# Performance work log

Measured on AMD Instinct MI355X. Metric: run time of the kernel, lower is better.

The kernel has to match this reference:

```python
import jax, jax.numpy as jnp
import numpy as np

M_HIST = 5        # Anderson history depth (m=5 in anderson_solver)
N_POWER = 20      # power iterations to estimate sigma for spectral_norm
REG = 1e-4        # Tikhonov regularization on the Anderson LS system
MAX_ITER = 25     # deq_max_iter


def _l2norm(x):
    return x / (jnp.linalg.norm(x) + 1e-12)


def spectral_normalize(W):
    # torch spectral_norm: W / sigma, sigma = u^T W v with u,v from power iteration
    u = _l2norm(jnp.ones((W.shape[0],), W.dtype))
    def body(_, u):
        v = _l2norm(W.T @ u)
        return _l2norm(W @ v)
    u = jax.lax.fori_loop(0, N_POWER, body, u)
    v = _l2norm(W.T @ u)
    u = jax.lax.stop_gradient(u)
    v = jax.lax.stop_gradient(v)
    sigma = u @ (W @ v)
    return W / sigma


def make_f(W1, b1, W2, b2):
    W1s = spectral_normalize(W1)
    W2s = spectral_normalize(W2)
    def f(z, context):
        h = jnp.tanh(jnp.concatenate([z, context], axis=-1) @ W1s.T + b1)
        return jnp.tanh(h @ W2s.T + b2)
    return f


def anderson(f, x0, context, max_iter, m=M_HIST):
    # Mirrors anderson_solver, including its duplicated warm-up step.
    X = [x0]
    F = [f(x0, context)]
    x = F[0]; X.append(x); F.append(f(x, context))
    x = F[0]; X.append(x); F.append(f(x, context))
    for _k in range(2, max_iter):
        m_k = min(len(X) - 1, m)
        dX = jnp.stack([X[-i] - X[-i - 1] for i in range(1, m_k + 1)], axis=-1)  # [B,d,mk]
        dF = jnp.stack([F[-i] - F[-i - 1] for i in range(1, m_k + 1)], axis=-1)
        dG = dF - dX
        A = jnp.einsum('bdi,bdj->bij', dG, dG) + REG * jnp.eye(m_k, dtype=x0.dtype)
        r = F[-1] - X[-1]
        Bv = jnp.einsum('bdi,bd->bi', dG, r)
        alpha = jnp.linalg.solve(A, Bv[..., None])[..., 0]          # [B,mk]
        x = F[-1] - jnp.einsum('bdi,bi->bd', dF, alpha)
        X.append(x)
        F.append(f(x, context))
        if len(X) > m + 1:
            X.pop(0); F.pop(0)
    return X[-1]


def setup_inputs() -> dict:
    key = jax.random.key(0)
    ks = jax.random.split(key, 5)
    B, X_DIM, LATENT, HIDDEN = 2048, 256, 256, 1024
    context = jax.random.normal(ks[0], (B, X_DIM), jnp.float32)
    W1 = jax.random.normal(ks[1], (HIDDEN, LATENT + X_DIM), jnp.float32) / np.sqrt(LATENT + X_DIM)
    b1 = jax.random.normal(ks[2], (HIDDEN,), jnp.float32) * 0.01
    W2 = jax.random.normal(ks[3], (LATENT, HIDDEN), jnp.float32) / np.sqrt(HIDDEN)
    b2 = jax.random.normal(ks[4], (LATENT,), jnp.float32) * 0.01
    return {"context": context, "W1": W1, "b1": b1, "W2": W2, "b2": b2}


def reference(context, W1, b1, W2, b2):
    f = make_f(W1, b1, W2, b2)
    z0 = jnp.zeros((context.shape[0], W2.shape[0]), context.dtype)
    z_star = anderson(f, z0, context, MAX_ITER)
    return z_star
```

## Files before the change

kernel.cpp:

```cpp
#include <hip/hip_runtime.h>
#include <hip/hip_bf16.h>


#define B_ROWS 2048
#define D_LAT  256
#define D_CTX  256
#define D_HID  1024
#define KCAT   512
#define SLOT   (B_ROWS * D_LAT)
#define NRING  7

typedef __bf16 bf16x8 __attribute__((ext_vector_type(8)));
typedef float f32x4 __attribute__((ext_vector_type(4)));
typedef float f32x2 __attribute__((ext_vector_type(2)));
typedef unsigned short u16;

__global__ void init_kernel(const float* __restrict__ ctx,
                            __hip_bfloat16* __restrict__ zc,
                            float* __restrict__ vA, float* __restrict__ uA,
                            float* __restrict__ G1p, float* __restrict__ G2) {
  int i = blockIdx.x * 256 + threadIdx.x;
  if (i < B_ROWS * KCAT) {
    int b = i >> 9, c = i & 511;
    float v = (c < 256) ? 0.0f : ctx[b * 256 + (c - 256)];
    zc[i] = __float2bfloat16(v);
  }
  if (i < 512 * 512) G1p[i] = 0.0f;
  if (i < 256 * 256) G2[i] = 0.0f;
  if (i < KCAT) vA[i] = 0.0f;
  if (i < D_LAT) uA[i] = 1.0f;
}

__global__ __launch_bounds__(256) void gram_kernel(
    const float* __restrict__ W1, const float* __restrict__ W2,
    float* __restrict__ G1p, float* __restrict__ G2) {
  __shared__ float As[32][66];
  __shared__ float Bs[32][34];
  const int tid = threadIdx.x;
  const int tx = tid & 15, ty = tid >> 4;

  const float* X; float* G; int N, ti, tj, k0base; bool modeA;
  int b = blockIdx.x;
  if (b < 1024) {
    modeA = true; X = W1; G = G1p; N = 512;
    int s = b >> 7, t = b & 127;
    ti = t >> 4; tj = t & 15; k0base = s * 128;
  } else {
    modeA = false; b -= 1024; X = W2; G = G2; N = 256;
    int s = b >> 5, t = b & 31;
    ti = t >> 3; tj = t & 7; k0base = s * 128;
  }

  float acc[4][2] = {};
  for (int k0 = k0base; k0 < k0base + 128; k0 += 32) {
    if (modeA) {
      for (int idx = tid; idx < 1024; idx += 256) {
        int r2 = (idx & 31) * 2, c = idx >> 5;
        f32x2 v = *(const f32x2*)(X + (size_t)(k0 + c) * 512 + ti * 64 + r2);
        *(f32x2*)&As[c][r2] = v;
      }
      for (int idx = tid; idx < 512; idx += 256) {
        int r2 = (idx & 15) * 2, c = idx >> 4;
        f32x2 v = *(const f32x2*)(X + (size_t)(k0 + c) * 512 + tj * 32 + r2);
        *(f32x2*)&Bs[c][r2] = v;
      }
    } else {
      for (int idx = tid; idx < 1024; idx += 256) {
        int c2 = (idx & 15) * 2, r = idx >> 4;
        f32x2 v = *(const f32x2*)(X + (size_t)(ti * 64 + r) * 1024 + k0 + c2);
        As[c2][r] = v[0];
        As[c2 + 1][r] = v[1];
      }
      for (int idx = tid; idx < 512; idx += 256) {
        int c2 = (idx & 15) * 2, r = idx >> 4;
        f32x2 v = *(const f32x2*)(X + (size_t)(tj * 32 + r) * 1024 + k0 + c2);
        Bs[c2][r] = v[0];
        Bs[c2 + 1][r] = v[1];
      }
    }
    __syncthreads();
#pragma unroll
    for (int kk = 0; kk < 32; kk++) {
      const float2* ap = (const float2*)&As[kk][ty * 4];
      float2 a0 = ap[0], a1 = ap[1];
      float2 b0 = *(const float2*)&Bs[kk][tx * 2];
      float a[4] = {a0.x, a0.y, a1.x, a1.y};
      float bb[2] = {b0.x, b0.y};
#pragma unroll
      for (int i = 0; i < 4; i++)
#pragma unroll
        for (int j = 0; j < 2; j++) acc[i][j] += a[i] * bb[j];
    }
    __syncthreads();
  }
#pragma unroll
  for (int i = 0; i < 4; i++)
#pragma unroll
    for (int j = 0; j < 2; j++)
      atomicAdd(&G[(size_t)(ti * 64 + ty * 4 + i) * N + tj * 32 + tx * 2 + j],
                acc[i][j]);
}

__global__ __launch_bounds__(256) void colsum_kernel(
    const float* __restrict__ W1, float* __restrict__ vA) {
  int b = blockIdx.x;
  for (int c = threadIdx.x; c < KCAT; c += 256) {
    float s = 0.f;
#pragma unroll
    for (int r = 0; r < 16; r++) s += W1[(size_t)(16 * b + r) * KCAT + c];
    atomicAdd(&vA[c], s);
  }
}

__global__ __launch_bounds__(256) void pmv_kernel(
    const float* __restrict__ G1p, const float* __restrict__ G2,
    const float* __restrict__ vi, float* __restrict__ vo,
    const float* __restrict__ ui, float* __restrict__ uo, int g1_active) {
  int gw = blockIdx.x * 4 + (threadIdx.x >> 6);
  int lane = threadIdx.x & 63;
  const float* G; const float* in; float* out; int n, r;
  if (gw < 512) {
    if (!g1_active) return;
    G = G1p; in = vi; out = vo; n = 512; r = gw;
  } else {
    G = G2; in = ui; out = uo; n = 256; r = gw - 512;
  }
  const float4* Gr = (const float4*)(G + (size_t)r * n);
  const float4* uv = (const float4*)in;
  float acc = 0.f;
  for (int c = lane; c < (n >> 2); c += 64) {
    float4 g = Gr[c], u = uv[c];
    acc += g.x * u.x + g.y * u.y + g.z * u.z + g.w * u.w;
  }
  for (int off = 32; off; off >>= 1) acc += __shfl_down(acc, off, 64);
  if (lane == 0) out[r] = 0.25f * acc;
}

__global__ __launch_bounds__(256) void sigma_kernel(
    const float* __restrict__ vA, const float* __restrict__ vB,
    const float* __restrict__ uA, const float* __restrict__ uB,
    float* __restrict__ sig) {
  float s[4] = {0.f, 0.f, 0.f, 0.f};
  for (int i = threadIdx.x; i < KCAT; i += 256) {
    s[0] += vA[i] * vB[i];
    s[1] += vA[i] * vA[i];
  }
  for (int i = threadIdx.x; i < D_LAT; i += 256) {
    s[2] += uA[i] * uA[i];
    s[3] += uA[i] * uB[i];
  }
  __shared__ float red[4][4];
  int lane = threadIdx.x & 63, w = threadIdx.x >> 6;
  for (int k = 0; k < 4; k++) {
    float a = s[k];
    for (int off = 32; off; off >>= 1) a += __shfl_down(a, off, 64);
    if (lane == 0) red[k][w] = a;
  }
  __syncthreads();
  if (threadIdx.x == 0) {
    float d0 = red[0][0] + red[0][1] + red[0][2] + red[0][3];
    float d1 = red[1][0] + red[1][1] + red[1][2] + red[1][3];
    float d2 = red[2][0] + red[2][1] + red[2][2] + red[2][3];
    float d3 = red[3][0] + red[3][1] + red[3][2] + red[3][3];
    sig[0] = sqrtf(0.25f * d0 / d1);
    sig[1] = sqrtf(0.25f * d2 / d3);
  }
}

__global__ void wfold_kernel(const float* __restrict__ W1,
                             const float* __restrict__ W2,
                             const float* __restrict__ sig,
                             __hip_bfloat16* __restrict__ W1b,
                             __hip_bfloat16* __restrict__ W2b) {
  int i = blockIdx.x * 256 + threadIdx.x;
  if (i < D_HID * KCAT) W1b[i] = __float2bfloat16(W1[i] * sig[0]);
  int j = i - D_HID * KCAT;
  if (j >= 0 && j < D_LAT * D_HID) W2b[j] = __float2bfloat16(W2[j] * sig[1]);
}

__global__ void warm1_kernel(const float* __restrict__ Fh,
                             float* __restrict__ Xh,
                             __hip_bfloat16* __restrict__ zc) {
  int i = blockIdx.x * 256 + threadIdx.x;
  float v = Fh[i];
  Xh[SLOT + i] = v;
  zc[(i >> 8) * KCAT + (i & 255)] = __float2bfloat16(v);
}
__global__ void warm2_kernel(const float* __restrict__ Fh,
                             float* __restrict__ Xh, float* __restrict__ Fw) {
  int i = blockIdx.x * 256 + threadIdx.x;
  Xh[2 * SLOT + i] = Fh[i];
  Fw[2 * SLOT + i] = Fh[SLOT + i];
}

template <int BM, int BN, int K, bool OUT_BF16>
__global__ __launch_bounds__(256) void gemm_mfma(
    const __hip_bfloat16* __restrict__ A, const __hip_bfloat16* __restrict__ W,
    const float* __restrict__ bias, float* __restrict__ Cf,
    __hip_bfloat16* __restrict__ Cb, int N) {
  __shared__ __align__(16) u16 lds[2][(BM + BN) * 64];
  const int tid = threadIdx.x;
  const int lane = tid & 63;
  const int wid = tid >> 6;
  const int wy = wid >> 1, wx = wid & 1;
  constexpr int WM = BM / 2, WN = BN / 2;
  constexpr int MB = WM / 16, NB = WN / 16;
  constexpr int NK = K / 64;
  const int bm = blockIdx.x * BM;
  const int bn = blockIdx.y * BN;
  const int rlo = lane & 15, quad = lane >> 4;

  f32x4 acc[MB][NB] = {};

  auto stage = [&](u16* base, int k0) {
    u16* As = base;
    u16* Ws = base + BM * 64;
    for (int c = tid; c < BM * 8; c += 256) {
      int r = c >> 3, o = (c & 7) ^ (r & 7);
      __builtin_amdgcn_global_load_lds(
          (const __attribute__((address_space(1))) void*)(A + (size_t)(bm + r) * K + k0 + o * 8),
          (__attribute__((address_space(3))) void*)(As + c * 8), 16, 0, 0);
    }
    for (int c = tid; c < BN * 8; c += 256) {
      int r = c >> 3, o = (c & 7) ^ (r & 7);
      __builtin_amdgcn_global_load_lds(
          (const __attribute__((address_space(1))) void*)(W + (size_t)(bn + r) * K + k0 + o * 8),
          (__attribute__((address_space(3))) void*)(Ws + c * 8), 16, 0, 0);
    }
  };
  auto compute = [&](const u16* base) {
    const u16* As = base;
    const u16* Ws = base + BM * 64;
#pragma unroll
    for (int kk = 0; kk < 2; kk++) {
      bf16x8 af[MB], bfr[NB];
#pragma unroll
      for (int mb = 0; mb < MB; mb++) {
        int r = wy * WM + mb * 16 + rlo;
        int o = (kk * 4 + quad) ^ (r & 7);
        af[mb] = *(const bf16x8*)(As + (r * 8 + o) * 8);
      }
#pragma unroll
      for (int nb = 0; nb < NB; nb++) {
        int r = wx * WN + nb * 16 + rlo;
        int o = (kk * 4 + quad) ^ (r & 7);
        bfr[nb] = *(const bf16x8*)(Ws + (r * 8 + o) * 8);
      }
#pragma unroll
      for (int mb = 0; mb < MB; mb++)
#pragma unroll
        for (int nb = 0; nb < NB; nb++)
          acc[mb][nb] = __builtin_amdgcn_mfma_f32_16x16x32_bf16(
              af[mb], bfr[nb], acc[mb][nb], 0, 0, 0);
    }
  };

  stage(&lds[0][0], 0);
  __syncthreads();
#pragma unroll 2
  for (int step = 0; step < NK; step++) {
    u16* cur = (step & 1) ? &lds[1][0] : &lds[0][0];
    u16* nxt = (step & 1) ? &lds[0][0] : &lds[1][0];
    if (step + 1 < NK) stage(nxt, (step + 1) * 64);
    compute(cur);
    if (step + 1 < NK) __syncthreads();
  }

#pragma unroll
  for (int mb = 0; mb < MB; mb++) {
#pragma unroll
    for (int nb = 0; nb < NB; nb++) {
      int n = bn + wx * WN + nb * 16 + rlo;
      float bv = bias[n];
#pragma unroll
      for (int rg = 0; rg < 4; rg++) {
        int m = bm + wy * WM + mb * 16 + quad * 4 + rg;
        float val = tanhf(acc[mb][nb][rg] + bv);
        if constexpr (OUT_BF16) {
          Cb[(size_t)m * N + n] = __float2bfloat16(val);
        } else {
          Cf[(size_t)m * N + n] = val;
        }
      }
    }
  }
}

template <int MK>
__global__ __launch_bounds__(256) void anderson_step_kernel(
    const float* __restrict__ Xh, const float* __restrict__ Fh,
    float* __restrict__ Xw, __hip_bfloat16* __restrict__ zc, int t) {
  const int lane = threadIdx.x & 63;
  const int wid = threadIdx.x >> 6;
  const int b = blockIdx.x * 4 + wid;
  const int base = b * D_LAT + 4 * lane;

  f32x4 f[MK + 1], x[MK + 1];
#pragma unroll
  for (int i = 0; i <= MK; i++) {
    int sl = (t - 1 - i) % NRING;
    f[i] = *(const f32x4*)(Fh + (size_t)sl * SLOT + base);
    x[i] = *(const f32x4*)(Xh + (size_t)sl * SLOT + base);
  }

  const f32x4 r = f[0] - x[0];
  f32x4 dF[MK], dG[MK];
#pragma unroll
  for (int i = 0; i < MK; i++) {
    dF[i] = f[i] - f[i + 1];
    dG[i] = dF[i] - (x[i] - x[i + 1]);
  }

  constexpr int NV = MK * (MK + 1) / 2 + MK;
  float vals[NV];
  {
    int p = 0;
#pragma unroll
    for (int i = 0; i < MK; i++)
#pragma unroll
      for (int j = i; j < MK; j++) {
        f32x4 q = dG[i] * dG[j];
        vals[p++] = q[0] + q[1] + q[2] + q[3];
      }
#pragma unroll
    for (int i = 0; i < MK; i++) {
      f32x4 q = dG[i] * r;
      vals[p++] = q[0] + q[1] + q[2] + q[3];
    }
  }
#pragma unroll
  for (int off = 1; off <= 32; off <<= 1)
#pragma unroll
    for (int v = 0; v < NV; v++) vals[v] += __shfl_xor(vals[v], off, 64);

  float A[MK][MK], bv[MK], alpha[MK];
  {
    int p = 0;
#pragma unroll
    for (int i = 0; i < MK; i++)
#pragma unroll
      for (int j = i; j < MK; j++) {
        A[i][j] = vals[p];
        A[j][i] = vals[p];
        p++;
      }
#pragma unroll
    for (int i = 0; i < MK; i++) A[i][i] += 1e-4f;
#pragma unroll
    for (int i = 0; i < MK; i++) bv[i] = vals[p++];
  }

#pragma unroll
  for (int c = 0; c < MK; c++) {
    float inv = 1.0f / A[c][c];
#pragma unroll
    for (int rr = c + 1; rr < MK; rr++) {
      float fct = A[rr][c] * inv;
#pragma unroll
      for (int cc = c; cc < MK; cc++) A[rr][cc] -= fct * A[c][cc];
      bv[rr] -= fct * bv[c];
    }
  }
#pragma unroll
  for (int i = MK - 1; i >= 0; i--) {
    float s = bv[i];
#pragma unroll
    for (int j = i + 1; j < MK; j++) s -= A[i][j] * alpha[j];
    alpha[i] = s / A[i][i];
  }

  f32x4 xo = f[0];
#pragma unroll
  for (int i = 0; i < MK; i++) xo -= dF[i] * alpha[i];
  *(f32x4*)(Xw + base) = xo;
  if (zc != nullptr) {
    union { __hip_bfloat16 h[4]; unsigned long long u; } cv;
#pragma unroll
    for (int j = 0; j < 4; j++) cv.h[j] = __float2bfloat16(xo[j]);
    *(unsigned long long*)(zc + (size_t)b * KCAT + 4 * lane) = cv.u;
  }
}

static void eval_f(const __hip_bfloat16* zc, const __hip_bfloat16* W1b,
                   const __hip_bfloat16* W2b, const float* b1, const float* b2,
                   __hip_bfloat16* hb, float* Fout, hipStream_t stream) {
  gemm_mfma<64, 64, KCAT, true><<<dim3(B_ROWS / 64, D_HID / 64), 256, 0,
                                  stream>>>(zc, W1b, b1, nullptr, hb, D_HID);
  gemm_mfma<32, 32, D_HID, false><<<dim3(B_ROWS / 32, D_LAT / 32), 256, 0,
                                    stream>>>(hb, W2b, b2, Fout, nullptr,
                                              D_LAT);
}

extern "C" void kernel_launch(void* const* d_in, const int* in_sizes, int n_in,
                              void* d_out, int out_size, void* d_ws,
                              size_t ws_size, hipStream_t stream) {
  const float* ctx = (const float*)d_in[0];
  const float* W1 = (const float*)d_in[1];
  const float* b1 = (const float*)d_in[2];
  const float* W2 = (const float*)d_in[3];
  const float* b2 = (const float*)d_in[4];
  float* out = (float*)d_out;

  float* ws = (float*)d_ws;
  float* sig = ws;
  float* vA = ws + 16;
  float* vB = vA + KCAT;
  float* uA = vB + KCAT;
  float* uB = uA + D_LAT;
  float* G1p = uB + D_LAT;
  float* G2 = G1p + KCAT * KCAT;
  float* Xh = G2 + D_LAT * D_LAT;
  float* Fh = Xh + NRING * SLOT;
  __hip_bfloat16* W1b = (__hip_bfloat16*)(Fh + NRING * SLOT);
  __hip_bfloat16* W2b = W1b + D_HID * KCAT;
  __hip_bfloat16* zc = W2b + D_LAT * D_HID;
  __hip_bfloat16* hb = zc + B_ROWS * KCAT;

  init_kernel<<<(B_ROWS * KCAT + 255) / 256, 256, 0, stream>>>(ctx, zc, vA, uA,
                                                               G1p, G2);
  gram_kernel<<<1280, 256, 0, stream>>>(W1, W2, G1p, G2);
  colsum_kernel<<<64, 256, 0, stream>>>(W1, vA);

  for (int it = 1; it <= 21; it++) {
    const float* vi; float* vo;
    const float* ui; float* uo;
    if (it & 1) { vi = vB; vo = vA; ui = uA; uo = uB; }
    else        { vi = vA; vo = vB; ui = uB; uo = uA; }
    pmv_kernel<<<192, 256, 0, stream>>>(G1p, G2, vi, vo, ui, uo, it >= 2);
  }
  sigma_kernel<<<1, 256, 0, stream>>>(vA, vB, uA, uB, sig);
  wfold_kernel<<<(D_HID * KCAT + D_LAT * D_HID + 255) / 256, 256, 0, stream>>>(
      W1, W2, sig, W1b, W2b);

  hipMemsetAsync(Xh, 0, SLOT * sizeof(float), stream);

  eval_f(zc, W1b, W2b, b1, b2, hb, Fh, stream);
  warm1_kernel<<<SLOT / 256, 256, 0, stream>>>(Fh, Xh, zc);
  eval_f(zc, W1b, W2b, b1, b2, hb, Fh + SLOT, stream);
  warm2_kernel<<<SLOT / 256, 256, 0, stream>>>(Fh, Xh, Fh);

  for (int t = 3; t <= 25; t++) {
    int mk = (t - 1 < 5) ? (t - 1) : 5;
    float* Xw = (t == 25) ? out : (Xh + (t % NRING) * SLOT);
    __hip_bfloat16* zarg = (t == 25) ? nullptr : zc;
    dim3 g(B_ROWS / 4);
    if (mk == 2)
      anderson_step_kernel<2><<<g, 256, 0, stream>>>(Xh, Fh, Xw, zarg, t);
    else if (mk == 3)
      anderson_step_kernel<3><<<g, 256, 0, stream>>>(Xh, Fh, Xw, zarg, t);
    else if (mk == 4)
      anderson_step_kernel<4><<<g, 256, 0, stream>>>(Xh, Fh, Xw, zarg, t);
    else
      anderson_step_kernel<5><<<g, 256, 0, stream>>>(Xh, Fh, Xw, zarg, t);
    if (t < 25) {
      eval_f(zc, W1b, W2b, b1, b2, hb, Fh + (t % NRING) * SLOT, stream);
    }
  }
}
```

Measured before the change: 768.8 us.

## Interleave F and X history into one ring layout and fuse colsum into gram

Stores each history slot as a single interleaved buffer where every 4 floats of F sit next to the matching 4 floats of X, so each Anderson-step thread reads both from one contiguous 32-byte span instead of two separate arrays. The second GEMM's epilogue writes directly into the interleaved layout, and the warm-up kernels and init are adjusted to match. The colsum kernel is folded into the gram kernel as extra blocks, and the memset is replaced by zeroing inside init. This saves a couple of launches and aims to improve access locality in the memory-bound Anderson step, at the cost of strided, half-filled stores in the GEMM epilogue.

```diff
diff --git a/kernel.cpp b/kernel.cpp
--- a/kernel.cpp
+++ b/kernel.cpp
@@ -8,6 +8,7 @@
 #define D_HID  1024
 #define KCAT   512
 #define SLOT   (B_ROWS * D_LAT)
+#define S2     (B_ROWS * 512)
 #define NRING  7
 
 typedef __bf16 bf16x8 __attribute__((ext_vector_type(8)));
@@ -18,13 +19,18 @@
 __global__ void init_kernel(const float* __restrict__ ctx,
                             __hip_bfloat16* __restrict__ zc,
                             float* __restrict__ vA, float* __restrict__ uA,
-                            float* __restrict__ G1p, float* __restrict__ G2) {
+                            float* __restrict__ G1p, float* __restrict__ G2,
+                            float* __restrict__ FXh) {
   int i = blockIdx.x * 256 + threadIdx.x;
   if (i < B_ROWS * KCAT) {
     int b = i >> 9, c = i & 511;
     float v = (c < 256) ? 0.0f : ctx[b * 256 + (c - 256)];
     zc[i] = __float2bfloat16(v);
   }
+  if (i < SLOT) {
+    int b = i >> 8, d = i & 255;
+    FXh[(size_t)b * 512 + ((d & ~3) << 1) + 4 + (d & 3)] = 0.0f;
+  }
   if (i < 512 * 512) G1p[i] = 0.0f;
   if (i < 256 * 256) G2[i] = 0.0f;
   if (i < KCAT) vA[i] = 0.0f;
@@ -33,14 +39,26 @@
 
 __global__ __launch_bounds__(256) void gram_kernel(
     const float* __restrict__ W1, const float* __restrict__ W2,
-    float* __restrict__ G1p, float* __restrict__ G2) {
+    float* __restrict__ G1p, float* __restrict__ G2,
+    float* __restrict__ vA) {
   __shared__ float As[32][66];
   __shared__ float Bs[32][34];
   const int tid = threadIdx.x;
   const int tx = tid & 15, ty = tid >> 4;
 
+  int b = blockIdx.x;
+  if (b >= 1280) {
+    int cb = b - 1280;
+    for (int c = tid; c < KCAT; c += 256) {
+      float s = 0.f;
+#pragma unroll
+      for (int r = 0; r < 16; r++) s += W1[(size_t)(16 * cb + r) * KCAT + c];
+      atomicAdd(&vA[c], s);
+    }
+    return;
+  }
+
   const float* X; float* G; int N, ti, tj, k0base; bool modeA;
-  int b = blockIdx.x;
   if (b < 1024) {
     modeA = true; X = W1; G = G1p; N = 512;
     int s = b >> 7, t = b & 127;
@@ -99,17 +117,6 @@
     for (int j = 0; j < 2; j++)
       atomicAdd(&G[(size_t)(ti * 64 + ty * 4 + i) * N + tj * 32 + tx * 2 + j],
                 acc[i][j]);
-}
-
-__global__ __launch_bounds__(256) void colsum_kernel(
-    const float* __restrict__ W1, float* __restrict__ vA) {
-  int b = blockIdx.x;
-  for (int c = threadIdx.x; c < KCAT; c += 256) {
-    float s = 0.f;
-#pragma unroll
-    for (int r = 0; r < 16; r++) s += W1[(size_t)(16 * b + r) * KCAT + c];
-    atomicAdd(&vA[c], s);
-  }
 }
 
 __global__ __launch_bounds__(256) void pmv_kernel(
@@ -178,22 +185,26 @@
   if (j >= 0 && j < D_LAT * D_HID) W2b[j] = __float2bfloat16(W2[j] * sig[1]);
 }
 
-__global__ void warm1_kernel(const float* __restrict__ Fh,
-                             float* __restrict__ Xh,
+__global__ void warm1_kernel(float* __restrict__ FXh,
                              __hip_bfloat16* __restrict__ zc) {
   int i = blockIdx.x * 256 + threadIdx.x;
-  float v = Fh[i];
-  Xh[SLOT + i] = v;
-  zc[(i >> 8) * KCAT + (i & 255)] = __float2bfloat16(v);
-}
-__global__ void warm2_kernel(const float* __restrict__ Fh,
-                             float* __restrict__ Xh, float* __restrict__ Fw) {
+  int b = i >> 8, d = i & 255;
+  size_t off = (size_t)b * 512 + ((d & ~3) << 1) + (d & 3);
+  float v = FXh[off];
+  FXh[S2 + off + 4] = v;
+  zc[b * KCAT + d] = __float2bfloat16(v);
+}
+__global__ void warm2_kernel(float* __restrict__ FXh) {
   int i = blockIdx.x * 256 + threadIdx.x;
-  Xh[2 * SLOT + i] = Fh[i];
-  Fw[2 * SLOT + i] = Fh[SLOT + i];
-}
-
-template <int BM, int BN, int K, bool OUT_BF16>
+  int b = i >> 8, d = i & 255;
+  size_t off = (size_t)b * 512 + ((d & ~3) << 1) + (d & 3);
+  float f0 = FXh[off];
+  float f1 = FXh[S2 + off];
+  FXh[2 * S2 + off + 4] = f0;
+  FXh[2 * S2 + off] = f1;
+}
+
+template <int BM, int BN, int K, int OUT_MODE>
 __global__ __launch_bounds__(256) void gemm_mfma(
     const __hip_bfloat16* __restrict__ A, const __hip_bfloat16* __restrict__ W,
     const float* __restrict__ bias, float* __restrict__ Cf,
@@ -276,31 +287,32 @@
       for (int rg = 0; rg < 4; rg++) {
         int m = bm + wy * WM + mb * 16 + quad * 4 + rg;
         float val = tanhf(acc[mb][nb][rg] + bv);
-        if constexpr (OUT_BF16) {
+        if constexpr (OUT_MODE == 0) {
           Cb[(size_t)m * N + n] = __float2bfloat16(val);
         } else {
-          Cf[(size_t)m * N + n] = val;
+          Cf[(size_t)m * 512 + ((n & ~3) << 1) + (n & 3)] = val;
         }
       }
     }
   }
 }
 
-template <int MK>
+template <int MK, bool LAST>
 __global__ __launch_bounds__(256) void anderson_step_kernel(
-    const float* __restrict__ Xh, const float* __restrict__ Fh,
-    float* __restrict__ Xw, __hip_bfloat16* __restrict__ zc, int t) {
+    float* __restrict__ FXh, float* __restrict__ out,
+    __hip_bfloat16* __restrict__ zc, int t) {
   const int lane = threadIdx.x & 63;
   const int wid = threadIdx.x >> 6;
   const int b = blockIdx.x * 4 + wid;
-  const int base = b * D_LAT + 4 * lane;
+  const size_t rowoff = (size_t)b * 512 + 8 * lane;
 
   f32x4 f[MK + 1], x[MK + 1];
 #pragma unroll
   for (int i = 0; i <= MK; i++) {
     int sl = (t - 1 - i) % NRING;
-    f[i] = *(const f32x4*)(Fh + (size_t)sl * SLOT + base);
-    x[i] = *(const f32x4*)(Xh + (size_t)sl * SLOT + base);
+    const float* p = FXh + (size_t)sl * S2 + rowoff;
+    f[i] = *(const f32x4*)p;
+    x[i] = *(const f32x4*)(p + 4);
   }
 
   const f32x4 r = f[0] - x[0];
@@ -372,8 +384,10 @@
   f32x4 xo = f[0];
 #pragma unroll
   for (int i = 0; i < MK; i++) xo -= dF[i] * alpha[i];
-  *(f32x4*)(Xw + base) = xo;
-  if (zc != nullptr) {
+  if constexpr (LAST) {
+    *(f32x4*)(out + (size_t)b * D_LAT + 4 * lane) = xo;
+  } else {
+    *(f32x4*)(FXh + (size_t)(t % NRING) * S2 + rowoff + 4) = xo;
     union { __hip_bfloat16 h[4]; unsigned long long u; } cv;
 #pragma unroll
     for (int j = 0; j < 4; j++) cv.h[j] = __float2bfloat16(xo[j]);
@@ -383,12 +397,11 @@
 
 static void eval_f(const __hip_bfloat16* zc, const __hip_bfloat16* W1b,
                    const __hip_bfloat16* W2b, const float* b1, const float* b2,
-                   __hip_bfloat16* hb, float* Fout, hipStream_t stream) {
-  gemm_mfma<64, 64, KCAT, true><<<dim3(B_ROWS / 64, D_HID / 64), 256, 0,
-                                  stream>>>(zc, W1b, b1, nullptr, hb, D_HID);
-  gemm_mfma<32, 32, D_HID, false><<<dim3(B_ROWS / 32, D_LAT / 32), 256, 0,
-                                    stream>>>(hb, W2b, b2, Fout, nullptr,
-                                              D_LAT);
+                   __hip_bfloat16* hb, float* FXslot, hipStream_t stream) {
+  gemm_mfma<64, 64, KCAT, 0><<<dim3(B_ROWS / 64, D_HID / 64), 256, 0,
+                               stream>>>(zc, W1b, b1, nullptr, hb, D_HID);
+  gemm_mfma<32, 32, D_HID, 1><<<dim3(B_ROWS / 32, D_LAT / 32), 256, 0,
+                                stream>>>(hb, W2b, b2, FXslot, nullptr, D_LAT);
 }
 
 extern "C" void kernel_launch(void* const* d_in, const int* in_sizes, int n_in,
@@ -409,17 +422,15 @@
   float* uB = uA + D_LAT;
   float* G1p = uB + D_LAT;
   float* G2 = G1p + KCAT * KCAT;
-  float* Xh = G2 + D_LAT * D_LAT;
-  float* Fh = Xh + NRING * SLOT;
-  __hip_bfloat16* W1b = (__hip_bfloat16*)(Fh + NRING * SLOT);
+  float* FXh = G2 + D_LAT * D_LAT;
+  __hip_bfloat16* W1b = (__hip_bfloat16*)(FXh + NRING * S2);
   __hip_bfloat16* W2b = W1b + D_HID * KCAT;
   __hip_bfloat16* zc = W2b + D_LAT * D_HID;
   __hip_bfloat16* hb = zc + B_ROWS * KCAT;
 
-  init_kernel<<<(B_ROWS * KCAT + 255) / 256, 256, 0, stream>>>(ctx, zc, vA, uA,
-                                                               G1p, G2);
-  gram_kernel<<<1280, 256, 0, stream>>>(W1, W2, G1p, G2);
-  colsum_kernel<<<64, 256, 0, stream>>>(W1, vA);
+  init_kernel<<<(B_ROWS * KCAT + 255) / 256, 256, 0, stream>>>(
+      ctx, zc, vA, uA, G1p, G2, FXh);
+  gram_kernel<<<1344, 256, 0, stream>>>(W1, W2, G1p, G2, vA);
 
   for (int it = 1; it <= 21; it++) {
     const float* vi; float* vo;
@@ -432,28 +443,26 @@
   wfold_kernel<<<(D_HID * KCAT + D_LAT * D_HID + 255) / 256, 256, 0, stream>>>(
       W1, W2, sig, W1b, W2b);
 
-  hipMemsetAsync(Xh, 0, SLOT * sizeof(float), stream);
-
-  eval_f(zc, W1b, W2b, b1, b2, hb, Fh, stream);
-  warm1_kernel<<<SLOT / 256, 256, 0, stream>>>(Fh, Xh, zc);
-  eval_f(zc, W1b, W2b, b1, b2, hb, Fh + SLOT, stream);
-  warm2_kernel<<<SLOT / 256, 256, 0, stream>>>(Fh, Xh, Fh);
+  eval_f(zc, W1b, W2b, b1, b2, hb, FXh, stream);
+  warm1_kernel<<<SLOT / 256, 256, 0, stream>>>(FXh, zc);
+  eval_f(zc, W1b, W2b, b1, b2, hb, FXh + S2, stream);
+  warm2_kernel<<<SLOT / 256, 256, 0, stream>>>(FXh);
 
   for (int t = 3; t <= 25; t++) {
     int mk = (t - 1 < 5) ? (t - 1) : 5;
-    float* Xw = (t == 25) ? out : (Xh + (t % NRING) * SLOT);
-    __hip_bfloat16* zarg = (t == 25) ? nullptr : zc;
     dim3 g(B_ROWS / 4);
-    if (mk == 2)
-      anderson_step_kernel<2><<<g, 256, 0, stream>>>(Xh, Fh, Xw, zarg, t);
-    else if (mk == 3)
-      anderson_step_kernel<3><<<g, 256, 0, stream>>>(Xh, Fh, Xw, zarg, t);
-    else if (mk == 4)
-      anderson_step_kernel<4><<<g, 256, 0, stream>>>(Xh, Fh, Xw, zarg, t);
-    else
-      anderson_step_kernel<5><<<g, 256, 0, stream>>>(Xh, Fh, Xw, zarg, t);
-    if (t < 25) {
-      eval_f(zc, W1b, W2b, b1, b2, hb, Fh + (t % NRING) * SLOT, stream);
-    }
-  }
-}
+    if (t == 25) {
+      anderson_step_kernel<5, true><<<g, 256, 0, stream>>>(FXh, out, nullptr, t);
+    } else {
+      if (mk == 2)
+        anderson_step_kernel<2, false><<<g, 256, 0, stream>>>(FXh, nullptr, zc, t);
+      else if (mk == 3)
+        anderson_step_kernel<3, false><<<g, 256, 0, stream>>>(FXh, nullptr, zc, t);
+      else if (mk == 4)
+        anderson_step_kernel<4, false><<<g, 256, 0, stream>>>(FXh, nullptr, zc, t);
+      else
+        anderson_step_kernel<5, false><<<g, 256, 0, stream>>>(FXh, nullptr, zc, t);
+      eval_f(zc, W1b, W2b, b1, b2, hb, FXh + (size_t)(t % NRING) * S2, stream);
+    }
+  }
+}
```

Measured after the change: 774.2 us. No clear change (+0.7%).
